# Kernel optimization log

Hardware: AMD Instinct MI355X
Metric: run time of the kernel (lower is better)

Reference implementation:

```python
import jax, jax.numpy as jnp
import numpy as np

H = 8
HD = 16  # head_dim = out_features // n_heads = 128 // 8


def setup_inputs() -> dict:
    key = jax.random.key(0)
    k1, k2, k3, k4, k5 = jax.random.split(key, 5)
    B, N, F_IN, F_OUT = 4, 2048, 128, 128
    x = jax.random.normal(k1, (B, N, F_IN), dtype=jnp.float32)
    adj = jax.random.randint(k2, (B, N, N), 0, 2, dtype=jnp.int32)
    W = jax.random.normal(k3, (F_IN, F_OUT), dtype=jnp.float32) * (1.0 / np.sqrt(F_IN))
    a = jax.random.normal(k4, (H, 2 * HD), dtype=jnp.float32) * 0.1
    Wo = jax.random.normal(k5, (F_OUT, F_OUT), dtype=jnp.float32) * (1.0 / np.sqrt(F_OUT))
    bo = jnp.zeros((F_OUT,), dtype=jnp.float32)
    return {"x": x, "adj": adj, "W": W, "a": a, "Wo": Wo, "bo": bo}


def reference(x, adj, W, a, Wo, bo):
    B, N, _ = x.shape
    # Linear projection (no bias), split heads: [B,H,N,HD]
    Wx = (x @ W).reshape(B, N, H, HD).transpose(0, 2, 1, 3)
    # Additive attention scores: e_ij = leaky(a_l . Wx_i + a_r . Wx_j)
    e_i = jnp.einsum('bhnd,hd->bhn', Wx, a[:, :HD])  # [B,H,N]
    e_j = jnp.einsum('bhnd,hd->bhn', Wx, a[:, HD:])  # [B,H,N]
    e = jax.nn.leaky_relu(e_i[:, :, :, None] + e_j[:, :, None, :], negative_slope=0.2)
    # Mask to edges of adj; rows with no edges -> all -inf -> softmax NaN -> 0
    mask = (adj[:, None, :, :] == 0)  # [B,1,N,N] broadcast over heads
    e = jnp.where(mask, -jnp.inf, e)
    attn = jax.nn.softmax(e, axis=-1)
    attn = jnp.nan_to_num(attn, nan=0.0)
    # Weighted aggregation, merge heads: [B,N,F_OUT]
    h = jnp.einsum('bhij,bhjd->bhid', attn, Wx)
    h = h.transpose(0, 2, 1, 3).reshape(B, N, H * HD)
    # out_proj (nn.Linear: y = h @ Wo.T + bo) then ELU
    return jax.nn.elu(h @ Wo.T + bo)
```

## Files before the change

### kernel.cpp

```cpp
#include <hip/hip_runtime.h>
#include <hip/hip_bf16.h>
#include <cstdint>


typedef float f32x2 __attribute__((ext_vector_type(2)));
typedef float f32x4 __attribute__((ext_vector_type(4)));
typedef __bf16 bf16x8 __attribute__((ext_vector_type(8)));
typedef unsigned long long u64;

__device__ __forceinline__ float lsel(float v, u64 m, u64 lanebit) {
#if __has_builtin(__builtin_amdgcn_inverse_ballot_w64)
    (void)lanebit;
    return __builtin_amdgcn_inverse_ballot_w64(m) ? v : 0.0f;
#else
    return (m & lanebit) ? v : 0.0f;
#endif
}

__global__ __launch_bounds__(256)
void prep_kernel(const float* __restrict__ x, const float* __restrict__ W,
                 const float* __restrict__ a, const float* __restrict__ Wo,
                 const int* __restrict__ adj,
                 unsigned short* __restrict__ wxT,
                 float2* __restrict__ EI,
                 float* __restrict__ EjT, float* __restrict__ Ej5T,
                 float* __restrict__ WoT,
                 u64* __restrict__ tmask)
{
    const int t = threadIdx.x;

    if (blockIdx.x < 2048) {
        __shared__ int al[16][257];
        const int blk2 = blockIdx.x;
        const int b = blk2 >> 9;
        const int tile = (blk2 >> 2) & 127;
        const int jq = blk2 & 3;
        const int rowbase = b * 2048 + tile * 16;
        const int w = t >> 6, lane = t & 63;
        const int r = lane & 15, jg = lane >> 4;
        const int srow = t >> 4, scol = (t & 15) * 16;

        #pragma unroll
        for (int cc = 0; cc < 2; ++cc) {
            const int jc = jq * 512 + cc * 256;
            const int* gsrc = adj + (size_t)(rowbase + srow) * 2048 + jc + scol;
            #pragma unroll
            for (int q = 0; q < 4; ++q) {
                const int4 v = *reinterpret_cast<const int4*>(&gsrc[q * 4]);
                al[srow][scol + q * 4 + 0] = v.x;
                al[srow][scol + q * 4 + 1] = v.y;
                al[srow][scol + q * 4 + 2] = v.z;
                al[srow][scol + q * 4 + 3] = v.w;
            }
            __syncthreads();
            u64 myw = 0;
            #pragma unroll
            for (int kk = 0; kk < 2; ++kk) {
                const int c0 = w * 64 + kk * 32 + jg * 8;
                const int4 a0 = *reinterpret_cast<const int4*>(&al[r][c0]);
                const int4 a1 = *reinterpret_cast<const int4*>(&al[r][c0 + 4]);
                const int av[8] = {a0.x, a0.y, a0.z, a0.w, a1.x, a1.y, a1.z, a1.w};
                #pragma unroll
                for (int e = 0; e < 8; ++e) {
                    const u64 bal = __ballot(av[e] != 0);
                    const int widx = kk * 8 + e;
                    if (lane == widx) myw = bal;
                }
            }
            __syncthreads();
            const int jtw = jq * 8 + cc * 4 + w;
            if (lane < 16)
                tmask[((size_t)(b * 128 + tile) * 32 + jtw) * 16 + lane] = myw;
        }
        return;
    }

    const int blk = blockIdx.x - 2048;
    if (blk == 1024) {
        if (t < 128)
            for (int k = 0; k < 128; ++k)
                WoT[k * 128 + t] = Wo[t * 128 + k];
        return;
    }
    __shared__ float xl[8 * 128];
    __shared__ float xw[8 * 128];
    const int row0 = blk * 8;
    if (t < 128) {
        #pragma unroll
        for (int r = 0; r < 8; ++r)
            xl[r * 128 + t] = x[(size_t)(row0 + r) * 128 + t];
    }
    __syncthreads();

    if (t < 128) {
        float acc[8] = {0.f, 0.f, 0.f, 0.f, 0.f, 0.f, 0.f, 0.f};
        for (int k = 0; k < 128; k += 4) {
            const float w0 = W[(k + 0) * 128 + t];
            const float w1 = W[(k + 1) * 128 + t];
            const float w2 = W[(k + 2) * 128 + t];
            const float w3 = W[(k + 3) * 128 + t];
            #pragma unroll
            for (int r = 0; r < 8; ++r) {
                const float4 xv = *reinterpret_cast<const float4*>(&xl[r * 128 + k]);
                acc[r] += xv.x * w0 + xv.y * w1 + xv.z * w2 + xv.w * w3;
            }
        }
        #pragma unroll
        for (int r = 0; r < 8; ++r) xw[r * 128 + t] = acc[r];
    }
    __syncthreads();

    if (t < 128) {
        const int b = row0 >> 11, n0 = row0 & 2047;
        bf16x8 st;
        #pragma unroll
        for (int r = 0; r < 8; ++r) st[r] = (__bf16)xw[r * 128 + t];
        *reinterpret_cast<bf16x8*>(&wxT[((size_t)(b * 128 + t)) * 2048 + n0]) = st;

        const int r = t >> 4, h = (t >> 1) & 7, s = t & 1;
        float dot = 0.f;
        #pragma unroll
        for (int d = 0; d < 16; ++d)
            dot += xw[r * 128 + h * 16 + d] * a[h * 32 + s * 16 + d];
        const float ef  = __expf(dot);
        const float ef5 = __expf(0.2f * dot);
        const int idx = (b * 8 + h) * 2048 + n0 + r;
        if (s) { EjT[idx] = ef; Ej5T[idx] = ef5; }
        else   { float2 ev; ev.x = ef; ev.y = ef5; EI[idx] = ev; }
    }
}

__global__ __launch_bounds__(512, 4)
void gat_kernel(const u64* __restrict__ tmask,
                const unsigned short* __restrict__ wxT,
                const float2* __restrict__ EI,
                const float* __restrict__ EjT, const float* __restrict__ Ej5T,
                const float* __restrict__ WoT, const float* __restrict__ bo,
                float* __restrict__ out)
{
    const int tid = threadIdx.x;
    const int h = tid >> 6;
    const int lane = tid & 63;
    const int r = lane & 15;
    const int jg = lane >> 4;
    const int jaof = jg * 8;
    const u64 lanebit = 1ull << lane;
    const int bid = (blockIdx.x & 7) * 64 + (blockIdx.x >> 3);
    const int b = bid >> 7;
    const int tile = bid & 127;
    const int ibase = tile << 4;

    __shared__ __align__(16) float EjL[2][8][128];
    __shared__ __align__(16) float Ej5L[2][8][128];
    __shared__ float hacc[16][128];

    const int eb = (b * 8 + h) * 2048;
    const float2 q0 = EI[eb + ibase + r];
    f32x2 EiE, Ei5E;
    EiE[0] = q0.x; EiE[1] = q0.x; Ei5E[0] = q0.y; Ei5E[1] = q0.y;
    const u64* tmrow = tmask + (size_t)(b * 128 + tile) * 512;

    const unsigned short* vrow = wxT + ((size_t)(b * 128 + h * 16 + r)) * 2048;
    const int jj = lane;
    const float* EjG  = EjT  + eb;
    const float* Ej5G = Ej5T + eb;

    f32x4 acc  = {0.f, 0.f, 0.f, 0.f};
    f32x4 accS = {0.f, 0.f, 0.f, 0.f};
    bf16x8 ones;
    #pragma unroll
    for (int e2 = 0; e2 < 8; ++e2) ones[e2] = (__bf16)1.0f;

    bf16x8 vC0, vC1, vC2, vC3, vN0, vN1, vN2, vN3;
    vC0 = *reinterpret_cast<const bf16x8*>(&vrow[jaof]);
    vC1 = *reinterpret_cast<const bf16x8*>(&vrow[32 + jaof]);
    vC2 = *reinterpret_cast<const bf16x8*>(&vrow[64 + jaof]);
    vC3 = *reinterpret_cast<const bf16x8*>(&vrow[96 + jaof]);
    {
        const float2 s0 = *reinterpret_cast<const float2*>(&EjG[jj * 2]);
        const float2 s1 = *reinterpret_cast<const float2*>(&Ej5G[jj * 2]);
        *reinterpret_cast<float2*>(&EjL[0][h][jj * 2]) = s0;
        *reinterpret_cast<float2*>(&Ej5L[0][h][jj * 2]) = s1;
    }
    __syncthreads();

    int cur = 0;
    for (int c = 0; c < 16; ++c) {
        const int jn = (c + 1) * 128;
        vN0 = *reinterpret_cast<const bf16x8*>(&vrow[jn + jaof]);
        vN1 = *reinterpret_cast<const bf16x8*>(&vrow[jn + 32 + jaof]);
        vN2 = *reinterpret_cast<const bf16x8*>(&vrow[jn + 64 + jaof]);
        vN3 = *reinterpret_cast<const bf16x8*>(&vrow[jn + 96 + jaof]);
        const float2 sn  = *reinterpret_cast<const float2*>(&EjG[jn + jj * 2]);
        const float2 sn5 = *reinterpret_cast<const float2*>(&Ej5G[jn + jj * 2]);
        __builtin_amdgcn_sched_barrier(0);

        const u64* tmw = tmrow + c * 32;
        u64 mwA[16], mwB[16];
        #pragma unroll
        for (int e2 = 0; e2 < 16; ++e2) mwA[e2] = tmw[e2];
        #pragma unroll
        for (int e2 = 0; e2 < 16; ++e2) mwB[e2] = tmw[16 + e2];

        #pragma unroll
        for (int kk = 0; kk < 4; ++kk) {
            const int jloc = kk * 32 + jaof;
            const float4 e0 = *reinterpret_cast<const float4*>(&EjL[cur][h][jloc]);
            const float4 e1 = *reinterpret_cast<const float4*>(&EjL[cur][h][jloc + 4]);
            const float4 f0 = *reinterpret_cast<const float4*>(&Ej5L[cur][h][jloc]);
            const float4 f1 = *reinterpret_cast<const float4*>(&Ej5L[cur][h][jloc + 4]);
            const bf16x8 v = (kk == 0) ? vC0 : (kk == 1) ? vC1 : (kk == 2) ? vC2 : vC3;
            const u64* mwp = (kk < 2) ? mwA : mwB;
            const int mof = (kk & 1) * 8;
            bf16x8 afr;
            #pragma unroll
            for (int ep = 0; ep < 4; ++ep) {
                const float4 ejv = (ep & 2) ? e1 : e0;
                const float4 ej5 = (ep & 2) ? f1 : f0;
                f32x2 ejp, ej5p;
                if (ep & 1) { ejp[0]=ejv.z; ejp[1]=ejv.w; ej5p[0]=ej5.z; ej5p[1]=ej5.w; }
                else        { ejp[0]=ejv.x; ejp[1]=ejv.y; ej5p[0]=ej5.x; ej5p[1]=ej5.y; }
                const f32x2 t1 = EiE * ejp;
                const f32x2 t2 = Ei5E * ej5p;
#if __has_builtin(__builtin_elementwise_max)
                const f32x2 tm2 = __builtin_elementwise_max(t1, t2);
#else
                f32x2 tm2; tm2[0] = fmaxf(t1[0], t2[0]); tm2[1] = fmaxf(t1[1], t2[1]);
#endif
                afr[2 * ep]     = (__bf16)lsel(tm2[0], mwp[mof + 2 * ep],     lanebit);
                afr[2 * ep + 1] = (__bf16)lsel(tm2[1], mwp[mof + 2 * ep + 1], lanebit);
            }
            acc  = __builtin_amdgcn_mfma_f32_16x16x32_bf16(afr, v,    acc,  0, 0, 0);
            accS = __builtin_amdgcn_mfma_f32_16x16x32_bf16(afr, ones, accS, 0, 0, 0);
        }

        const int nb = cur ^ 1;
        *reinterpret_cast<float2*>(&EjL[nb][h][jj * 2]) = sn;
        *reinterpret_cast<float2*>(&Ej5L[nb][h][jj * 2]) = sn5;
        __syncthreads();
        vC0 = vN0; vC1 = vN1; vC2 = vN2; vC3 = vN3;
        cur = nb;
    }

    #pragma unroll
    for (int q = 0; q < 4; ++q) {
        const int row = jg * 4 + q;
        const float inv = (accS[q] > 0.f) ? 1.f / accS[q] : 0.f;
        hacc[row][h * 16 + r] = acc[q] * inv;
    }
    __syncthreads();

    const int f = tid & 127;
    const int rg = tid >> 7;
    float o0 = 0.f, o1 = 0.f, o2 = 0.f, o3 = 0.f;
    for (int k = 0; k < 128; k += 4) {
        const float w0 = WoT[(k + 0) * 128 + f];
        const float w1 = WoT[(k + 1) * 128 + f];
        const float w2 = WoT[(k + 2) * 128 + f];
        const float w3 = WoT[(k + 3) * 128 + f];
        const float4 h0 = *reinterpret_cast<const float4*>(&hacc[rg * 4 + 0][k]);
        const float4 h1 = *reinterpret_cast<const float4*>(&hacc[rg * 4 + 1][k]);
        const float4 h2v = *reinterpret_cast<const float4*>(&hacc[rg * 4 + 2][k]);
        const float4 h3 = *reinterpret_cast<const float4*>(&hacc[rg * 4 + 3][k]);
        o0 += h0.x * w0 + h0.y * w1 + h0.z * w2 + h0.w * w3;
        o1 += h1.x * w0 + h1.y * w1 + h1.z * w2 + h1.w * w3;
        o2 += h2v.x * w0 + h2v.y * w1 + h2v.z * w2 + h2v.w * w3;
        o3 += h3.x * w0 + h3.y * w1 + h3.z * w2 + h3.w * w3;
    }
    const float bv = bo[f];
    float vv[4] = {o0 + bv, o1 + bv, o2 + bv, o3 + bv};
    #pragma unroll
    for (int q = 0; q < 4; ++q) {
        float v = vv[q];
        v = (v > 0.f) ? v : (__expf(v) - 1.f);
        out[(size_t)(b * 2048 + ibase + rg * 4 + q) * 128 + f] = v;
    }
}

extern "C" void kernel_launch(void* const* d_in, const int* in_sizes, int n_in,
                              void* d_out, int out_size, void* d_ws, size_t ws_size,
                              hipStream_t stream) {
    const float* x   = (const float*)d_in[0];
    const int*   adj = (const int*)d_in[1];
    const float* W   = (const float*)d_in[2];
    const float* a   = (const float*)d_in[3];
    const float* Wo  = (const float*)d_in[4];
    const float* bo  = (const float*)d_in[5];
    float* out = (float*)d_out;

    char* ws = (char*)d_ws;
    unsigned short* wxT = (unsigned short*)ws;
    float2* EI  = (float2*)(ws + (size_t)2 * 1024 * 1024);
    float* EjT  = (float*)(EI + 4 * 8 * 2048);
    float* Ej5T = EjT + 4 * 8 * 2048;
    float* WoT  = Ej5T + 4 * 8 * 2048;
    u64* tmask = (u64*)(WoT + 128 * 128);

    prep_kernel<<<dim3(2048 + 1025), dim3(256), 0, stream>>>(
        x, W, a, Wo, adj, wxT, EI, EjT, Ej5T, WoT, tmask);
    gat_kernel<<<dim3(512), dim3(512), 0, stream>>>(
        tmask, wxT, EI, EjT, Ej5T, WoT, bo, out);
}
```

Measured before the change: 72.38 us.

## Split neighbor dimension across two wave groups per block with shared reduction

Doubles the block to 1024 threads so two sets of 8 waves each process half of the 2048 neighbor columns. Partial numerators and softmax denominators are combined through shared memory before normalization, and the output projection is spread over twice as many threads. The aim is more waves in flight per block and a shorter serial loop per wave, which should hide more latency. The cost is an extra shared-memory reduction and barrier. The launch bound of 1024 threads with 8 blocks per CU may also constrain register allocation.

```diff
diff --git a/kernel.cpp b/kernel.cpp
--- a/kernel.cpp
+++ b/kernel.cpp
@@ -130,7 +130,7 @@
     }
 }
 
-__global__ __launch_bounds__(512, 4)
+__global__ __launch_bounds__(1024, 8)
 void gat_kernel(const u64* __restrict__ tmask,
                 const unsigned short* __restrict__ wxT,
                 const float2* __restrict__ EI,
@@ -139,7 +139,9 @@
                 float* __restrict__ out)
 {
     const int tid = threadIdx.x;
-    const int h = tid >> 6;
+    const int w = tid >> 6;
+    const int h = w & 7;
+    const int jh = w >> 3;
     const int lane = tid & 63;
     const int r = lane & 15;
     const int jg = lane >> 4;
@@ -150,11 +152,13 @@
     const int tile = bid & 127;
     const int ibase = tile << 4;
 
-    __shared__ __align__(16) float EjL[2][8][128];
-    __shared__ __align__(16) float Ej5L[2][8][128];
+    __shared__ __align__(16) float EjL[2][2][8][128];
+    __shared__ __align__(16) float Ej5L[2][2][8][128];
     __shared__ float hacc[16][128];
+    __shared__ float hsum[8][16];
 
     const int eb = (b * 8 + h) * 2048;
+    const int jbase = jh * 1024;
     const float2 q0 = EI[eb + ibase + r];
     f32x2 EiE, Ei5E;
     EiE[0] = q0.x; EiE[1] = q0.x; Ei5E[0] = q0.y; Ei5E[1] = q0.y;
@@ -172,21 +176,21 @@
     for (int e2 = 0; e2 < 8; ++e2) ones[e2] = (__bf16)1.0f;
 
     bf16x8 vC0, vC1, vC2, vC3, vN0, vN1, vN2, vN3;
-    vC0 = *reinterpret_cast<const bf16x8*>(&vrow[jaof]);
-    vC1 = *reinterpret_cast<const bf16x8*>(&vrow[32 + jaof]);
-    vC2 = *reinterpret_cast<const bf16x8*>(&vrow[64 + jaof]);
-    vC3 = *reinterpret_cast<const bf16x8*>(&vrow[96 + jaof]);
+    vC0 = *reinterpret_cast<const bf16x8*>(&vrow[jbase + jaof]);
+    vC1 = *reinterpret_cast<const bf16x8*>(&vrow[jbase + 32 + jaof]);
+    vC2 = *reinterpret_cast<const bf16x8*>(&vrow[jbase + 64 + jaof]);
+    vC3 = *reinterpret_cast<const bf16x8*>(&vrow[jbase + 96 + jaof]);
     {
-        const float2 s0 = *reinterpret_cast<const float2*>(&EjG[jj * 2]);
-        const float2 s1 = *reinterpret_cast<const float2*>(&Ej5G[jj * 2]);
-        *reinterpret_cast<float2*>(&EjL[0][h][jj * 2]) = s0;
-        *reinterpret_cast<float2*>(&Ej5L[0][h][jj * 2]) = s1;
+        const float2 s0 = *reinterpret_cast<const float2*>(&EjG[jbase + jj * 2]);
+        const float2 s1 = *reinterpret_cast<const float2*>(&Ej5G[jbase + jj * 2]);
+        *reinterpret_cast<float2*>(&EjL[jh][0][h][jj * 2]) = s0;
+        *reinterpret_cast<float2*>(&Ej5L[jh][0][h][jj * 2]) = s1;
     }
     __syncthreads();
 
     int cur = 0;
-    for (int c = 0; c < 16; ++c) {
-        const int jn = (c + 1) * 128;
+    for (int c = 0; c < 8; ++c) {
+        const int jn = jbase + (c + 1) * 128;
         vN0 = *reinterpret_cast<const bf16x8*>(&vrow[jn + jaof]);
         vN1 = *reinterpret_cast<const bf16x8*>(&vrow[jn + 32 + jaof]);
         vN2 = *reinterpret_cast<const bf16x8*>(&vrow[jn + 64 + jaof]);
@@ -195,7 +199,7 @@
         const float2 sn5 = *reinterpret_cast<const float2*>(&Ej5G[jn + jj * 2]);
         __builtin_amdgcn_sched_barrier(0);
 
-        const u64* tmw = tmrow + c * 32;
+        const u64* tmw = tmrow + (jh * 16 + c * 2) * 16;
         u64 mwA[16], mwB[16];
         #pragma unroll
         for (int e2 = 0; e2 < 16; ++e2) mwA[e2] = tmw[e2];
@@ -205,10 +209,10 @@
         #pragma unroll
         for (int kk = 0; kk < 4; ++kk) {
             const int jloc = kk * 32 + jaof;
-            const float4 e0 = *reinterpret_cast<const float4*>(&EjL[cur][h][jloc]);
-            const float4 e1 = *reinterpret_cast<const float4*>(&EjL[cur][h][jloc + 4]);
-            const float4 f0 = *reinterpret_cast<const float4*>(&Ej5L[cur][h][jloc]);
-            const float4 f1 = *reinterpret_cast<const float4*>(&Ej5L[cur][h][jloc + 4]);
+            const float4 e0 = *reinterpret_cast<const float4*>(&EjL[jh][cur][h][jloc]);
+            const float4 e1 = *reinterpret_cast<const float4*>(&EjL[jh][cur][h][jloc + 4]);
+            const float4 f0 = *reinterpret_cast<const float4*>(&Ej5L[jh][cur][h][jloc]);
+            const float4 f1 = *reinterpret_cast<const float4*>(&Ej5L[jh][cur][h][jloc + 4]);
             const bf16x8 v = (kk == 0) ? vC0 : (kk == 1) ? vC1 : (kk == 2) ? vC2 : vC3;
             const u64* mwp = (kk < 2) ? mwA : mwB;
             const int mof = (kk & 1) * 8;
@@ -235,45 +239,55 @@
         }
 
         const int nb = cur ^ 1;
-        *reinterpret_cast<float2*>(&EjL[nb][h][jj * 2]) = sn;
-        *reinterpret_cast<float2*>(&Ej5L[nb][h][jj * 2]) = sn5;
+        *reinterpret_cast<float2*>(&EjL[jh][nb][h][jj * 2]) = sn;
+        *reinterpret_cast<float2*>(&Ej5L[jh][nb][h][jj * 2]) = sn5;
         __syncthreads();
         vC0 = vN0; vC1 = vN1; vC2 = vN2; vC3 = vN3;
         cur = nb;
     }
 
-    #pragma unroll
-    for (int q = 0; q < 4; ++q) {
-        const int row = jg * 4 + q;
-        const float inv = (accS[q] > 0.f) ? 1.f / accS[q] : 0.f;
-        hacc[row][h * 16 + r] = acc[q] * inv;
+    if (jh == 1) {
+        #pragma unroll
+        for (int q = 0; q < 4; ++q)
+            hacc[jg * 4 + q][h * 16 + r] = acc[q];
+        if (r == 0) {
+            #pragma unroll
+            for (int q = 0; q < 4; ++q) hsum[h][jg * 4 + q] = accS[q];
+        }
+    }
+    __syncthreads();
+    if (jh == 0) {
+        #pragma unroll
+        for (int q = 0; q < 4; ++q) {
+            const int row = jg * 4 + q;
+            const float num = acc[q] + hacc[row][h * 16 + r];
+            const float den = accS[q] + hsum[h][row];
+            const float inv = (den > 0.f) ? 1.f / den : 0.f;
+            hacc[row][h * 16 + r] = num * inv;
+        }
     }
     __syncthreads();
 
     const int f = tid & 127;
     const int rg = tid >> 7;
-    float o0 = 0.f, o1 = 0.f, o2 = 0.f, o3 = 0.f;
+    float o0 = 0.f, o1 = 0.f;
     for (int k = 0; k < 128; k += 4) {
         const float w0 = WoT[(k + 0) * 128 + f];
         const float w1 = WoT[(k + 1) * 128 + f];
         const float w2 = WoT[(k + 2) * 128 + f];
         const float w3 = WoT[(k + 3) * 128 + f];
-        const float4 h0 = *reinterpret_cast<const float4*>(&hacc[rg * 4 + 0][k]);
-        const float4 h1 = *reinterpret_cast<const float4*>(&hacc[rg * 4 + 1][k]);
-        const float4 h2v = *reinterpret_cast<const float4*>(&hacc[rg * 4 + 2][k]);
-        const float4 h3 = *reinterpret_cast<const float4*>(&hacc[rg * 4 + 3][k]);
+        const float4 h0 = *reinterpret_cast<const float4*>(&hacc[rg * 2 + 0][k]);
+        const float4 h1 = *reinterpret_cast<const float4*>(&hacc[rg * 2 + 1][k]);
         o0 += h0.x * w0 + h0.y * w1 + h0.z * w2 + h0.w * w3;
         o1 += h1.x * w0 + h1.y * w1 + h1.z * w2 + h1.w * w3;
-        o2 += h2v.x * w0 + h2v.y * w1 + h2v.z * w2 + h2v.w * w3;
-        o3 += h3.x * w0 + h3.y * w1 + h3.z * w2 + h3.w * w3;
     }
     const float bv = bo[f];
-    float vv[4] = {o0 + bv, o1 + bv, o2 + bv, o3 + bv};
+    float vv[2] = {o0 + bv, o1 + bv};
     #pragma unroll
-    for (int q = 0; q < 4; ++q) {
+    for (int q = 0; q < 2; ++q) {
         float v = vv[q];
         v = (v > 0.f) ? v : (__expf(v) - 1.f);
-        out[(size_t)(b * 2048 + ibase + rg * 4 + q) * 128 + f] = v;
+        out[(size_t)(b * 2048 + ibase + rg * 2 + q) * 128 + f] = v;
     }
 }
 
@@ -298,6 +312,6 @@
 
     prep_kernel<<<dim3(2048 + 1025), dim3(256), 0, stream>>>(
         x, W, a, Wo, adj, wxT, EI, EjT, Ej5T, WoT, tmask);
-    gat_kernel<<<dim3(512), dim3(512), 0, stream>>>(
+    gat_kernel<<<dim3(512), dim3(1024), 0, stream>>>(
         tmask, wxT, EI, EjT, Ej5T, WoT, bo, out);
 }
```

After: 190.8 us. 164% more time.

## Split attention over neighbor halves and head groups, combine in separate kernel

Applied to the files above, without the earlier changes.

The single fused attention kernel becomes a split-K style gat_part kernel and a combine kernel. gat_part runs 2048 blocks of 256 threads, each handling four heads and half of the neighbor range, and writes partial numerators and softmax denominators to workspace. It reads Ej and V straight from global memory, dropping the LDS double buffering and per-chunk syncs. The combine kernel sums the two halves, normalizes, and applies the output projection and ELU. This adds more parallelism and occupancy, at the cost of an extra launch and a partial-sum round trip through global memory.

```diff
diff --git a/kernel.cpp b/kernel.cpp
--- a/kernel.cpp
+++ b/kernel.cpp
@@ -130,40 +130,37 @@
     }
 }
 
-__global__ __launch_bounds__(512, 4)
-void gat_kernel(const u64* __restrict__ tmask,
-                const unsigned short* __restrict__ wxT,
-                const float2* __restrict__ EI,
-                const float* __restrict__ EjT, const float* __restrict__ Ej5T,
-                const float* __restrict__ WoT, const float* __restrict__ bo,
-                float* __restrict__ out)
+__global__ __launch_bounds__(256, 8)
+void gat_part(const u64* __restrict__ tmask,
+              const unsigned short* __restrict__ wxT,
+              const float2* __restrict__ EI,
+              const float* __restrict__ EjT, const float* __restrict__ Ej5T,
+              float* __restrict__ pacc, float* __restrict__ psum)
 {
     const int tid = threadIdx.x;
-    const int h = tid >> 6;
+    const int hw = tid >> 6;
     const int lane = tid & 63;
     const int r = lane & 15;
     const int jg = lane >> 4;
     const int jaof = jg * 8;
     const u64 lanebit = 1ull << lane;
-    const int bid = (blockIdx.x & 7) * 64 + (blockIdx.x >> 3);
-    const int b = bid >> 7;
-    const int tile = bid & 127;
+    const int x = blockIdx.x & 7, w = blockIdx.x >> 3;
+    const int tg = x * 64 + (w & 63);
+    const int sub = w >> 6;
+    const int jh = sub >> 1, hg = sub & 1;
+    const int b = tg >> 7;
+    const int tile = tg & 127;
     const int ibase = tile << 4;
-
-    __shared__ __align__(16) float EjL[2][8][128];
-    __shared__ __align__(16) float Ej5L[2][8][128];
-    __shared__ float hacc[16][128];
+    const int h = hg * 4 + hw;
 
     const int eb = (b * 8 + h) * 2048;
     const float2 q0 = EI[eb + ibase + r];
     f32x2 EiE, Ei5E;
     EiE[0] = q0.x; EiE[1] = q0.x; Ei5E[0] = q0.y; Ei5E[1] = q0.y;
-    const u64* tmrow = tmask + (size_t)(b * 128 + tile) * 512;
-
+    const float* EjR  = EjT  + eb;
+    const float* Ej5R = Ej5T + eb;
     const unsigned short* vrow = wxT + ((size_t)(b * 128 + h * 16 + r)) * 2048;
-    const int jj = lane;
-    const float* EjG  = EjT  + eb;
-    const float* Ej5G = Ej5T + eb;
+    const u64* tmrow = tmask + (size_t)(b * 128 + tile) * 512 + jh * 256;
 
     f32x4 acc  = {0.f, 0.f, 0.f, 0.f};
     f32x4 accS = {0.f, 0.f, 0.f, 0.f};
@@ -171,47 +168,23 @@
     #pragma unroll
     for (int e2 = 0; e2 < 8; ++e2) ones[e2] = (__bf16)1.0f;
 
-    bf16x8 vC0, vC1, vC2, vC3, vN0, vN1, vN2, vN3;
-    vC0 = *reinterpret_cast<const bf16x8*>(&vrow[jaof]);
-    vC1 = *reinterpret_cast<const bf16x8*>(&vrow[32 + jaof]);
-    vC2 = *reinterpret_cast<const bf16x8*>(&vrow[64 + jaof]);
-    vC3 = *reinterpret_cast<const bf16x8*>(&vrow[96 + jaof]);
-    {
-        const float2 s0 = *reinterpret_cast<const float2*>(&EjG[jj * 2]);
-        const float2 s1 = *reinterpret_cast<const float2*>(&Ej5G[jj * 2]);
-        *reinterpret_cast<float2*>(&EjL[0][h][jj * 2]) = s0;
-        *reinterpret_cast<float2*>(&Ej5L[0][h][jj * 2]) = s1;
-    }
-    __syncthreads();
-
-    int cur = 0;
+    const int jbase = jh * 1024;
     for (int c = 0; c < 16; ++c) {
-        const int jn = (c + 1) * 128;
-        vN0 = *reinterpret_cast<const bf16x8*>(&vrow[jn + jaof]);
-        vN1 = *reinterpret_cast<const bf16x8*>(&vrow[jn + 32 + jaof]);
-        vN2 = *reinterpret_cast<const bf16x8*>(&vrow[jn + 64 + jaof]);
-        vN3 = *reinterpret_cast<const bf16x8*>(&vrow[jn + 96 + jaof]);
-        const float2 sn  = *reinterpret_cast<const float2*>(&EjG[jn + jj * 2]);
-        const float2 sn5 = *reinterpret_cast<const float2*>(&Ej5G[jn + jj * 2]);
-        __builtin_amdgcn_sched_barrier(0);
-
-        const u64* tmw = tmrow + c * 32;
-        u64 mwA[16], mwB[16];
-        #pragma unroll
-        for (int e2 = 0; e2 < 16; ++e2) mwA[e2] = tmw[e2];
-        #pragma unroll
-        for (int e2 = 0; e2 < 16; ++e2) mwB[e2] = tmw[16 + e2];
-
-        #pragma unroll
-        for (int kk = 0; kk < 4; ++kk) {
-            const int jloc = kk * 32 + jaof;
-            const float4 e0 = *reinterpret_cast<const float4*>(&EjL[cur][h][jloc]);
-            const float4 e1 = *reinterpret_cast<const float4*>(&EjL[cur][h][jloc + 4]);
-            const float4 f0 = *reinterpret_cast<const float4*>(&Ej5L[cur][h][jloc]);
-            const float4 f1 = *reinterpret_cast<const float4*>(&Ej5L[cur][h][jloc + 4]);
-            const bf16x8 v = (kk == 0) ? vC0 : (kk == 1) ? vC1 : (kk == 2) ? vC2 : vC3;
-            const u64* mwp = (kk < 2) ? mwA : mwB;
-            const int mof = (kk & 1) * 8;
+        const int j0 = jbase + c * 64;
+        const u64* tmw = tmrow + c * 16;
+        u64 mw[16];
+        #pragma unroll
+        for (int e2 = 0; e2 < 16; ++e2) mw[e2] = tmw[e2];
+
+        #pragma unroll
+        for (int kk = 0; kk < 2; ++kk) {
+            const int ja = j0 + kk * 32 + jaof;
+            const float4 e0 = *reinterpret_cast<const float4*>(&EjR[ja]);
+            const float4 e1 = *reinterpret_cast<const float4*>(&EjR[ja + 4]);
+            const float4 f0 = *reinterpret_cast<const float4*>(&Ej5R[ja]);
+            const float4 f1 = *reinterpret_cast<const float4*>(&Ej5R[ja + 4]);
+            const bf16x8 v = *reinterpret_cast<const bf16x8*>(&vrow[ja]);
+            const int mof = kk * 8;
             bf16x8 afr;
             #pragma unroll
             for (int ep = 0; ep < 4; ++ep) {
@@ -227,53 +200,74 @@
 #else
                 f32x2 tm2; tm2[0] = fmaxf(t1[0], t2[0]); tm2[1] = fmaxf(t1[1], t2[1]);
 #endif
-                afr[2 * ep]     = (__bf16)lsel(tm2[0], mwp[mof + 2 * ep],     lanebit);
-                afr[2 * ep + 1] = (__bf16)lsel(tm2[1], mwp[mof + 2 * ep + 1], lanebit);
+                afr[2 * ep]     = (__bf16)lsel(tm2[0], mw[mof + 2 * ep],     lanebit);
+                afr[2 * ep + 1] = (__bf16)lsel(tm2[1], mw[mof + 2 * ep + 1], lanebit);
             }
             acc  = __builtin_amdgcn_mfma_f32_16x16x32_bf16(afr, v,    acc,  0, 0, 0);
             accS = __builtin_amdgcn_mfma_f32_16x16x32_bf16(afr, ones, accS, 0, 0, 0);
         }
-
-        const int nb = cur ^ 1;
-        *reinterpret_cast<float2*>(&EjL[nb][h][jj * 2]) = sn;
-        *reinterpret_cast<float2*>(&Ej5L[nb][h][jj * 2]) = sn5;
-        __syncthreads();
-        vC0 = vN0; vC1 = vN1; vC2 = vN2; vC3 = vN3;
-        cur = nb;
-    }
-
+    }
+
+    const size_t pb = (size_t)((b * 128 + tile) * 2 + jh);
+    float* pa = pacc + pb * 2048;
+    float* ps = psum + pb * 128;
     #pragma unroll
     for (int q = 0; q < 4; ++q) {
         const int row = jg * 4 + q;
-        const float inv = (accS[q] > 0.f) ? 1.f / accS[q] : 0.f;
-        hacc[row][h * 16 + r] = acc[q] * inv;
+        pa[row * 128 + hg * 64 + hw * 16 + r] = acc[q];
+        if (r == 0) ps[(hg * 4 + hw) * 16 + row] = accS[q];
+    }
+}
+
+__global__ __launch_bounds__(256)
+void combine_kernel(const float* __restrict__ pacc, const float* __restrict__ psum,
+                    const float* __restrict__ WoT, const float* __restrict__ bo,
+                    float* __restrict__ out)
+{
+    const int tid = threadIdx.x;
+    const int bid = (blockIdx.x & 7) * 64 + (blockIdx.x >> 3);
+    const int b = bid >> 7;
+    const int tile = bid & 127;
+    const int ibase = tile << 4;
+
+    __shared__ float hl[16][128];
+    const size_t pb0 = (size_t)((b * 128 + tile) * 2);
+    const float* pa0 = pacc + pb0 * 2048;
+    const float* pa1 = pa0 + 2048;
+    const float* ps0 = psum + pb0 * 128;
+    const float* ps1 = ps0 + 128;
+
+    #pragma unroll
+    for (int k = 0; k < 8; ++k) {
+        const int idx = k * 256 + tid;
+        const int row = idx >> 7, f = idx & 127, h = f >> 4;
+        const float num = pa0[idx] + pa1[idx];
+        const float den = ps0[h * 16 + row] + ps1[h * 16 + row];
+        const float inv = (den > 0.f) ? 1.f / den : 0.f;
+        hl[row][f] = num * inv;
     }
     __syncthreads();
 
     const int f = tid & 127;
     const int rg = tid >> 7;
-    float o0 = 0.f, o1 = 0.f, o2 = 0.f, o3 = 0.f;
+    float o[8] = {0.f, 0.f, 0.f, 0.f, 0.f, 0.f, 0.f, 0.f};
     for (int k = 0; k < 128; k += 4) {
         const float w0 = WoT[(k + 0) * 128 + f];
         const float w1 = WoT[(k + 1) * 128 + f];
         const float w2 = WoT[(k + 2) * 128 + f];
         const float w3 = WoT[(k + 3) * 128 + f];
-        const float4 h0 = *reinterpret_cast<const float4*>(&hacc[rg * 4 + 0][k]);
-        const float4 h1 = *reinterpret_cast<const float4*>(&hacc[rg * 4 + 1][k]);
-        const float4 h2v = *reinterpret_cast<const float4*>(&hacc[rg * 4 + 2][k]);
-        const float4 h3 = *reinterpret_cast<const float4*>(&hacc[rg * 4 + 3][k]);
-        o0 += h0.x * w0 + h0.y * w1 + h0.z * w2 + h0.w * w3;
-        o1 += h1.x * w0 + h1.y * w1 + h1.z * w2 + h1.w * w3;
-        o2 += h2v.x * w0 + h2v.y * w1 + h2v.z * w2 + h2v.w * w3;
-        o3 += h3.x * w0 + h3.y * w1 + h3.z * w2 + h3.w * w3;
+        #pragma unroll
+        for (int q = 0; q < 8; ++q) {
+            const float4 hv = *reinterpret_cast<const float4*>(&hl[rg * 8 + q][k]);
+            o[q] += hv.x * w0 + hv.y * w1 + hv.z * w2 + hv.w * w3;
+        }
     }
     const float bv = bo[f];
-    float vv[4] = {o0 + bv, o1 + bv, o2 + bv, o3 + bv};
     #pragma unroll
-    for (int q = 0; q < 4; ++q) {
-        float v = vv[q];
+    for (int q = 0; q < 8; ++q) {
+        float v = o[q] + bv;
         v = (v > 0.f) ? v : (__expf(v) - 1.f);
-        out[(size_t)(b * 2048 + ibase + rg * 4 + q) * 128 + f] = v;
+        out[(size_t)(b * 2048 + ibase + rg * 8 + q) * 128 + f] = v;
     }
 }
 
@@ -295,9 +289,13 @@
     float* Ej5T = EjT + 4 * 8 * 2048;
     float* WoT  = Ej5T + 4 * 8 * 2048;
     u64* tmask = (u64*)(WoT + 128 * 128);
+    float* pacc = (float*)(tmask + (size_t)512 * 512);
+    float* psum = pacc + (size_t)1024 * 2048;
 
     prep_kernel<<<dim3(2048 + 1025), dim3(256), 0, stream>>>(
         x, W, a, Wo, adj, wxT, EI, EjT, Ej5T, WoT, tmask);
-    gat_kernel<<<dim3(512), dim3(512), 0, stream>>>(
-        tmask, wxT, EI, EjT, Ej5T, WoT, bo, out);
-}
+    gat_part<<<dim3(2048), dim3(256), 0, stream>>>(
+        tmask, wxT, EI, EjT, Ej5T, pacc, psum);
+    combine_kernel<<<dim3(512), dim3(256), 0, stream>>>(
+        pacc, psum, WoT, bo, out);
+}
```

Result: slower. 108.7 us (+50.2%).
